# Kernel tuning notes

Measured on AMD Instinct MI355X. Metric: run time of the kernel, lower is better.

The kernel has to match this reference:

```python
import jax, jax.numpy as jnp
import numpy as np
from jax import lax

B, N = 4, 5  # batches, cavs per batch (record_len fixed to 5)
SHAPES = [(64, 128, 256), (128, 64, 128), (256, 32, 64)]  # (C,H,W) per scale


def _base_grid(H, W, align_corners):
    if align_corners:
        xs = jnp.linspace(-1.0, 1.0, W)
        ys = jnp.linspace(-1.0, 1.0, H)
    else:
        xs = (jnp.arange(W, dtype=jnp.float32) + 0.5) * (2.0 / W) - 1.0
        ys = (jnp.arange(H, dtype=jnp.float32) + 0.5) * (2.0 / H) - 1.0
    gx, gy = jnp.meshgrid(xs, ys)  # [H,W] each, x varies along W
    return jnp.stack([gx, gy], axis=-1)  # [H,W,2]


def affine_grid(theta, H, W, align_corners):
    # theta: [M,2,3]  -> grid [M,H,W,2], matches torch.F.affine_grid
    base = _base_grid(H, W, align_corners)
    coords = jnp.concatenate([base, jnp.ones((H, W, 1), base.dtype)], axis=-1)  # [H,W,3]
    return jnp.einsum('nij,hwj->nhwi', theta, coords)


def grid_sample(img, grid, align_corners):
    # img [M,C,H,W], grid [M,Hg,Wg,2]; bilinear, zero padding (torch defaults)
    M, C, H, W = img.shape
    gx, gy = grid[..., 0], grid[..., 1]
    if align_corners:
        ix = (gx + 1.0) * 0.5 * (W - 1)
        iy = (gy + 1.0) * 0.5 * (H - 1)
    else:
        ix = ((gx + 1.0) * W - 1.0) * 0.5
        iy = ((gy + 1.0) * H - 1.0) * 0.5
    x0 = jnp.floor(ix); y0 = jnp.floor(iy)
    x1 = x0 + 1.0;      y1 = y0 + 1.0
    wx1 = ix - x0; wx0 = 1.0 - wx1
    wy1 = iy - y0; wy0 = 1.0 - wy1

    def sample_corner(im, xx, yy):
        valid = ((xx >= 0) & (xx < W) & (yy >= 0) & (yy < H)).astype(im.dtype)
        xc = jnp.clip(xx, 0, W - 1).astype(jnp.int32)
        yc = jnp.clip(yy, 0, H - 1).astype(jnp.int32)
        return im[:, yc, xc] * valid[None]  # [C,Hg,Wg]

    def per_image(im, x0_, x1_, y0_, y1_, w00, w01, w10, w11):
        return (sample_corner(im, x0_, y0_) * w00[None]
                + sample_corner(im, x1_, y0_) * w01[None]
                + sample_corner(im, x0_, y1_) * w10[None]
                + sample_corner(im, x1_, y1_) * w11[None])

    return jax.vmap(per_image)(img, x0, x1, y0, y1, wx0 * wy0, wx1 * wy0, wx0 * wy1, wx1 * wy1)


def conv2d(x, w, b, pad):
    y = lax.conv_general_dilated(x, w, (1, 1), [(pad, pad), (pad, pad)],
                                 dimension_numbers=('NCHW', 'OIHW', 'NCHW'))
    return y + b[None, :, None, None]


def instance_norm(x, eps=1e-5):  # torch InstanceNorm2d(affine=False)
    m = jnp.mean(x, axis=(2, 3), keepdims=True)
    v = jnp.var(x, axis=(2, 3), keepdims=True)
    return (x - m) * lax.rsqrt(v + eps)


def leaky(x):
    return jnp.where(x >= 0, x, 0.01 * x)


def setup_inputs():
    key = jax.random.key(0)
    ks = jax.random.split(key, 8)
    out = {}
    for i, (C, H, W) in enumerate(SHAPES):
        out[f'feat{i}'] = jax.random.normal(ks[i], (B * N, C, H, W), dtype=jnp.float32)
    eye = jnp.array([[1., 0., 0.], [0., 1., 0.]], dtype=jnp.float32)
    out['pairwise_t_matrix'] = (jnp.broadcast_to(eye, (B, N, N, 2, 3))
                                + 0.02 * jax.random.normal(ks[3], (B, N, N, 2, 3), dtype=jnp.float32))
    out['record_len'] = jnp.full((B,), N, dtype=jnp.int32)
    C0 = SHAPES[0][0]
    def w(k, shape, fan):
        return jax.random.normal(k, shape, jnp.float32) * (1.0 / np.sqrt(fan))
    out['w1'] = w(ks[4], (32, 2 * C0, 3, 3), 2 * C0 * 9); out['b1'] = jnp.zeros((32,), jnp.float32)
    out['w2'] = w(ks[5], (16, 32, 3, 3), 32 * 9);          out['b2'] = jnp.zeros((16,), jnp.float32)
    out['w3'] = w(ks[6], (8, 16, 1, 1), 16);               out['b3'] = jnp.zeros((8,), jnp.float32)
    out['w4'] = w(ks[7], (2, 8, 1, 1), 8) * 0.1;           out['b4'] = jnp.zeros((2,), jnp.float32)
    return out


def _forward(feat0, feat1, feat2, pairwise_t_matrix, w1, b1, w2, b2, w3, b3, w4, b4):
    feats = [feat0, feat1, feat2]
    # warp every agent into ego (i=0) frame at every scale; warp_affine_simple uses align_corners=True
    theta = pairwise_t_matrix[:, 0, :, :, :].reshape(B * N, 2, 3)
    warped = []
    for f in feats:
        C, H, W = f.shape[1:]
        g = affine_grid(theta, H, W, True)
        warped.append(grid_sample(f, g, True).reshape(B, N, C, H, W))
    C0, H0, W0 = feats[0].shape[1:]
    w0 = warped[0]
    ego = jnp.broadcast_to(w0[:, :1], (B, N - 1, C0, H0, W0))
    cat = jnp.concatenate([ego, w0[:, 1:]], axis=2).reshape(B * (N - 1), 2 * C0, H0, W0)
    # ArbitraryOffset grid net
    x = leaky(instance_norm(conv2d(cat, w1, b1, 1)))
    x = leaky(instance_norm(conv2d(x, w2, b2, 1)))
    x = leaky(instance_norm(conv2d(x, w3, b3, 0)))
    x = conv2d(x, w4, b4, 0)  # [M,2,H0,W0]
    grid_res = x.reshape(B * (N - 1), H0, W0, 2)  # faithful: raw reshape as in the torch source
    grid = grid_res + _base_grid(H0, W0, False)   # identity affine_grid (align_corners=False)
    fused = []
    for s, f in enumerate(warped):
        C, Hs, Ws = f.shape[2:]
        gs = grid[:, ::2 ** s, ::2 ** s, :]  # [M,Hs,Ws,2]
        neigh = f[:, 1:].reshape(B * (N - 1), C, Hs, Ws)
        deformed = grid_sample(neigh, gs, False).reshape(B, N - 1, C, Hs, Ws)
        fused.append(jnp.max(jnp.concatenate([deformed, f[:, :1]], axis=1), axis=1))
    return tuple(fused)


def reference(feat0, feat1, feat2, pairwise_t_matrix, record_len, w1, b1, w2, b2, w3, b3, w4, b4):
    # record_len is fixed to N per batch (constant); kept for signature fidelity
    return _forward(feat0, feat1, feat2, pairwise_t_matrix, w1, b1, w2, b2, w3, b3, w4, b4)
```

## Files before the change

### kernel.cpp

```cpp
#include <hip/hip_runtime.h>


struct Bilin { int i00, i01, i10, i11; float w00, w01, w10, w11; };

__device__ __forceinline__ Bilin make_bilin(float ix, float iy, int W, int H) {
    float x0f = floorf(ix), y0f = floorf(iy);
    float wx1 = ix - x0f, wy1 = iy - y0f;
    float wx0 = 1.f - wx1, wy0 = 1.f - wy1;
    int x0 = (int)x0f, y0 = (int)y0f;
    int x1 = x0 + 1, y1 = y0 + 1;
    bool vx0 = (x0 >= 0 && x0 < W), vx1 = (x1 >= 0 && x1 < W);
    bool vy0 = (y0 >= 0 && y0 < H), vy1 = (y1 >= 0 && y1 < H);
    int cx0 = min(max(x0, 0), W - 1), cx1 = min(max(x1, 0), W - 1);
    int cy0 = min(max(y0, 0), H - 1), cy1 = min(max(y1, 0), H - 1);
    Bilin b;
    b.i00 = cy0 * W + cx0; b.i01 = cy0 * W + cx1;
    b.i10 = cy1 * W + cx0; b.i11 = cy1 * W + cx1;
    b.w00 = (vx0 && vy0) ? wx0 * wy0 : 0.f;
    b.w01 = (vx1 && vy0) ? wx1 * wy0 : 0.f;
    b.w10 = (vx0 && vy1) ? wx0 * wy1 : 0.f;
    b.w11 = (vx1 && vy1) ? wx1 * wy1 : 0.f;
    return b;
}

__device__ __forceinline__ Bilin affine_bilin(const float* th, int xq, int yq, int W, int H) {
    float gx = -1.f + 2.f * xq / (float)(W - 1);
    float gy = -1.f + 2.f * yq / (float)(H - 1);
    float tx = th[0] * gx + th[1] * gy + th[2];
    float ty = th[3] * gx + th[4] * gy + th[5];
    float ix = (tx + 1.f) * 0.5f * (W - 1);
    float iy = (ty + 1.f) * 0.5f * (H - 1);
    return make_bilin(ix, iy, W, H);
}

__global__ __launch_bounds__(256) void warp_kernel(
    const float* __restrict__ src, const float* __restrict__ tmat,
    float* __restrict__ dst, int C, int H, int W)
{
    int idx = blockIdx.x * 256 + threadIdx.x;
    int CGn = C >> 4;
    int HW = H * W;
    int total = 20 * CGn * HW;
    if (idx >= total) return;
    int w   = idx % W;
    int h   = (idx / W) % H;
    int cg  = (idx / HW) % CGn;
    int img = idx / (HW * CGn);
    int b = img / 5, n = img % 5;
    const float* th = tmat + (b * 25 + n) * 6;
    float gx = -1.f + 2.f * w / (float)(W - 1);
    float gy = -1.f + 2.f * h / (float)(H - 1);
    float tx = th[0] * gx + th[1] * gy + th[2];
    float ty = th[3] * gx + th[4] * gy + th[5];
    float ix = (tx + 1.f) * 0.5f * (W - 1);
    float iy = (ty + 1.f) * 0.5f * (H - 1);
    Bilin bl = make_bilin(ix, iy, W, H);
    const float* im = src + ((size_t)img * C + cg * 16) * HW;
    float* op = dst + ((size_t)img * C + cg * 16) * HW + h * W + w;
    #pragma unroll 4
    for (int c = 0; c < 16; ++c) {
        const float* pl = im + c * HW;
        op[c * HW] = pl[bl.i00] * bl.w00 + pl[bl.i01] * bl.w01 +
                     pl[bl.i10] * bl.w10 + pl[bl.i11] * bl.w11;
    }
}

__global__ void zero_stats(float* s) {
    for (int i = threadIdx.x; i < 1792; i += 256) s[i] = 0.f;
}

__global__ void finalize_stats(float* s, int n, float inv_hw) {
    int i = threadIdx.x;
    if (i < n) {
        float m = s[2 * i] * inv_hw;
        float v = s[2 * i + 1] * inv_hw - m * m;
        s[2 * i]     = m;
        s[2 * i + 1] = rsqrtf(v + 1e-5f);
    }
}

__global__ void transpose_w(const float* __restrict__ w1, const float* __restrict__ w2,
                            float* __restrict__ wt1, float* __restrict__ wt2) {
    int t = blockIdx.x * 256 + threadIdx.x;
    for (int i = t; i < 128 * 9 * 32; i += 32 * 256) {
        int o = i % 32, pos = (i / 32) % 9, cin = i / 288;
        wt1[i] = w1[o * 1152 + cin * 9 + pos];
    }
    for (int i = t; i < 32 * 9 * 16; i += 32 * 256) {
        int o = i % 16, pos = (i / 16) % 9, cin = i / 144;
        wt2[i] = w2[o * 288 + cin * 9 + pos];
    }
}

template<int CIN, int COUT, int SRC, bool INIT, bool NORM, bool STATS>
__global__ __launch_bounds__(256, 2) void conv3x3v3(
    const float* __restrict__ src, const float* __restrict__ wt,
    const float* __restrict__ bias, const float* __restrict__ stats,
    const float* __restrict__ init, float* __restrict__ dst,
    float* __restrict__ statacc)
{
    constexpr int H = 128, W = 256, HW = H * W;
    constexpr int CHUNK = 8, NCH = CIN / CHUNK;
    constexpr int OCP = COUT / 4;
    constexpr int PW = 68;
    __shared__ __align__(16) float s_in[CHUNK][10][PW];

    int tid = threadIdx.x, bi = blockIdx.x;
    int p = bi >> 6, rem = bi & 63;
    int h_base = (rem >> 2) * 8;
    int w_base = (rem & 3) * 64;
    int cg = tid >> 6, sg = tid & 63;
    int r = sg & 7, cw = (sg >> 3) * 8;
    int cg_u = __builtin_amdgcn_readfirstlane(cg);

    const float* base;
    if (SRC == 1)      base = src + (size_t)(p * 5) * 64 * HW;
    else if (SRC == 2) { int bb = p >> 2, jm = p & 3; base = src + (size_t)((bb * 5 + 1 + jm) * 64) * HW; }
    else               base = src + (size_t)p * CIN * HW;

    int gofs[3], lofs[3];
    unsigned pvm = 0, ivm = 0;
    #pragma unroll
    for (int k = 0; k < 3; ++k) {
        int e = tid + k * 256;
        bool pv = (e < 660);
        int row = e / 66, col = e % 66;
        int gy = h_base + row - 1, gx = w_base + col - 1;
        bool iv = pv && gy >= 0 && gy < H && gx >= 0 && gx < W;
        gofs[k] = iv ? (gy * W + gx) : 0;
        lofs[k] = pv ? (row * PW + col) : 0;
        pvm |= (pv ? 1u : 0u) << k;
        ivm |= (iv ? 1u : 0u) << k;
    }
    float* lds = &s_in[0][0][0];

    float acc[OCP][8];
    #pragma unroll
    for (int o = 0; o < OCP; ++o)
        #pragma unroll
        for (int i = 0; i < 8; ++i) acc[o][i] = 0.f;

    float pf[3][CHUNK];
    #pragma unroll
    for (int k = 0; k < 3; ++k)
        if (pvm >> k & 1)
            #pragma unroll
            for (int c = 0; c < CHUNK; ++c)
                pf[k][c] = base[(size_t)c * HW + gofs[k]];

    for (int ci = 0; ci < NCH; ++ci) {
        if (ci) __syncthreads();
        float mrs[NORM ? 2 * CHUNK : 1];
        if (NORM) {
            const float4* sp = (const float4*)(stats + (size_t)(p * CIN + ci * CHUNK) * 2);
            #pragma unroll
            for (int q = 0; q < CHUNK / 2; ++q) {
                float4 v = sp[q];
                mrs[q * 4] = v.x; mrs[q * 4 + 1] = v.y; mrs[q * 4 + 2] = v.z; mrs[q * 4 + 3] = v.w;
            }
        }
        #pragma unroll
        for (int k = 0; k < 3; ++k) {
            if (pvm >> k & 1) {
                #pragma unroll
                for (int c = 0; c < CHUNK; ++c) {
                    float v = (ivm >> k & 1) ? pf[k][c] : 0.f;
                    if (NORM && (ivm >> k & 1)) {
                        v = (v - mrs[2 * c]) * mrs[2 * c + 1];
                        v = v >= 0.f ? v : 0.01f * v;
                    }
                    lds[c * (10 * PW) + lofs[k]] = v;
                }
            }
        }
        __syncthreads();
        if (ci + 1 < NCH) {
            const float* nb = base + (size_t)(ci + 1) * CHUNK * HW;
            #pragma unroll
            for (int k = 0; k < 3; ++k)
                if (pvm >> k & 1)
                    #pragma unroll
                    for (int c = 0; c < CHUNK; ++c)
                        pf[k][c] = nb[(size_t)c * HW + gofs[k]];
        }
        #pragma unroll 1
        for (int c = 0; c < CHUNK; ++c) {
            float in[3][10];
            #pragma unroll
            for (int dy = 0; dy < 3; ++dy) {
                const float* rp = &s_in[c][r + dy][cw];
                float4 a = *reinterpret_cast<const float4*>(rp);
                float4 b = *reinterpret_cast<const float4*>(rp + 4);
                float2 e = *reinterpret_cast<const float2*>(rp + 8);
                in[dy][0] = a.x; in[dy][1] = a.y; in[dy][2] = a.z; in[dy][3] = a.w;
                in[dy][4] = b.x; in[dy][5] = b.y; in[dy][6] = b.z; in[dy][7] = b.w;
                in[dy][8] = e.x; in[dy][9] = e.y;
            }
            const float* wp = wt + (size_t)((ci * CHUNK + c) * 9) * COUT + cg_u * OCP;
            #pragma unroll
            for (int pos = 0; pos < 9; ++pos) {
                const int dy = pos / 3, dx = pos % 3;
                float wv[OCP];
                #pragma unroll
                for (int oq = 0; oq < OCP; oq += 4) {
                    float4 wq = *reinterpret_cast<const float4*>(wp + pos * COUT + oq);
                    wv[oq] = wq.x; wv[oq + 1] = wq.y; wv[oq + 2] = wq.z; wv[oq + 3] = wq.w;
                }
                #pragma unroll
                for (int o = 0; o < OCP; ++o)
                    #pragma unroll
                    for (int px = 0; px < 8; ++px)
                        acc[o][px] = fmaf(in[dy][dx + px], wv[o], acc[o][px]);
            }
        }
    }
    int hh = h_base + r, ww = w_base + cw;
    #pragma unroll
    for (int o = 0; o < OCP; ++o) {
        int oc = cg * OCP + o;
        float bv = (SRC == 1) ? 0.f : bias[oc];
        float add[8];
        #pragma unroll
        for (int i = 0; i < 8; ++i) add[i] = bv;
        if (INIT) {
            int bb = (SRC == 2) ? (p >> 2) : p;
            const float* ip = init + ((size_t)bb * COUT + oc) * HW + hh * W + ww;
            float4 e0 = *reinterpret_cast<const float4*>(ip);
            float4 e1 = *reinterpret_cast<const float4*>(ip + 4);
            add[0] += e0.x; add[1] += e0.y; add[2] += e0.z; add[3] += e0.w;
            add[4] += e1.x; add[5] += e1.y; add[6] += e1.z; add[7] += e1.w;
        }
        float vals[8];
        #pragma unroll
        for (int i = 0; i < 8; ++i) vals[i] = acc[o][i] + add[i];
        float* op = dst + (((size_t)p * COUT + oc) * H + hh) * W + ww;
        *reinterpret_cast<float4*>(op)     = make_float4(vals[0], vals[1], vals[2], vals[3]);
        *reinterpret_cast<float4*>(op + 4) = make_float4(vals[4], vals[5], vals[6], vals[7]);
        if (STATS) {
            float s = 0.f, s2 = 0.f;
            #pragma unroll
            for (int i = 0; i < 8; ++i) { s += vals[i]; s2 += vals[i] * vals[i]; }
            #pragma unroll
            for (int off = 32; off > 0; off >>= 1) {
                s  += __shfl_down(s, off);
                s2 += __shfl_down(s2, off);
            }
            if (sg == 0) {
                atomicAdd(&statacc[(size_t)(p * COUT + oc) * 2],     s);
                atomicAdd(&statacc[(size_t)(p * COUT + oc) * 2 + 1], s2);
            }
        }
    }
}

template<int CIN, int COUT, bool STATS>
__global__ __launch_bounds__(256) void conv1x1_kernel(
    const float* __restrict__ src, const float* __restrict__ wgt,
    const float* __restrict__ bias, const float* __restrict__ stats,
    float* __restrict__ dst, float* __restrict__ statacc)
{
    constexpr int HW = 128 * 256;
    __shared__ float s_w[COUT * CIN];
    __shared__ float s_b[COUT];
    __shared__ float s_part[4][2 * COUT];
    int tid = threadIdx.x;
    for (int t = tid; t < COUT * CIN; t += 256) s_w[t] = wgt[t];
    if (tid < COUT) s_b[tid] = bias[tid];
    __syncthreads();
    int p  = blockIdx.x >> 7;
    int px = ((blockIdx.x & 127) << 8) + tid;
    float in[CIN];
    #pragma unroll
    for (int c = 0; c < CIN; ++c) {
        float v  = src[((size_t)p * CIN + c) * HW + px];
        float m  = stats[(p * CIN + c) * 2];
        float rs = stats[(p * CIN + c) * 2 + 1];
        v = (v - m) * rs;
        in[c] = v >= 0.f ? v : 0.01f * v;
    }
    float val[COUT];
    #pragma unroll
    for (int o = 0; o < COUT; ++o) {
        float s = s_b[o];
        #pragma unroll
        for (int c = 0; c < CIN; ++c) s = fmaf(in[c], s_w[o * CIN + c], s);
        val[o] = s;
        dst[((size_t)p * COUT + o) * HW + px] = s;
    }
    if (STATS) {
        int wv = tid >> 6, ln = tid & 63;
        #pragma unroll
        for (int o = 0; o < COUT; ++o) {
            float s = val[o], s2 = val[o] * val[o];
            #pragma unroll
            for (int off = 32; off > 0; off >>= 1) {
                s  += __shfl_down(s, off);
                s2 += __shfl_down(s2, off);
            }
            if (ln == 0) { s_part[wv][o * 2] = s; s_part[wv][o * 2 + 1] = s2; }
        }
        __syncthreads();
        if (tid < 2 * COUT) {
            float t = s_part[0][tid] + s_part[1][tid] + s_part[2][tid] + s_part[3][tid];
            atomicAdd(&statacc[(size_t)p * COUT * 2 + tid], t);
        }
    }
}

__global__ __launch_bounds__(256) void fuse0_kernel(
    const float* __restrict__ W0, const float* __restrict__ grid,
    float* __restrict__ out)
{
    constexpr int HW = 32768;
    constexpr int CPT = 16;
    int bid = blockIdx.x;
    int swz = (bid & 7) * 256 + (bid >> 3);
    int idx = swz * 256 + threadIdx.x;
    int px = idx & 32767;
    int cg = (idx >> 15) & 3;
    int b  = idx >> 17;
    int w = px & 255, h = px >> 8;
    float bx = (w + 0.5f) * (2.f / 256.f) - 1.f;
    float by = (h + 0.5f) * (2.f / 128.f) - 1.f;
    Bilin bl[4];
    #pragma unroll
    for (int j = 0; j < 4; ++j) {
        const float2 g = *reinterpret_cast<const float2*>(
            grid + ((size_t)(b * 4 + j)) * 65536 + (size_t)px * 2);
        float ix = ((g.x + bx + 1.f) * 256.f - 1.f) * 0.5f;
        float iy = ((g.y + by + 1.f) * 128.f - 1.f) * 0.5f;
        bl[j] = make_bilin(ix, iy, 256, 128);
    }
    const float* ego = W0 + ((size_t)(b * 5) * 64 + cg * CPT) * HW + px;
    float* op = out + ((size_t)b * 64 + cg * CPT) * HW + px;
    #pragma unroll 2
    for (int c = 0; c < CPT; ++c) {
        float mx = ego[(size_t)c * HW];
        #pragma unroll
        for (int j = 0; j < 4; ++j) {
            const float* pl = W0 + ((size_t)(b * 5 + 1 + j) * 64 + cg * CPT + c) * HW;
            float s = pl[bl[j].i00] * bl[j].w00 + pl[bl[j].i01] * bl[j].w01 +
                      pl[bl[j].i10] * bl[j].w10 + pl[bl[j].i11] * bl[j].w11;
            mx = fmaxf(mx, s);
        }
        op[(size_t)c * HW] = mx;
    }
}

template<int C, int CPT, int SH, int HS, int WS>
__global__ __launch_bounds__(256) void fuse_comp(
    const float* __restrict__ feat, const float* __restrict__ tmat,
    const float* __restrict__ grid, float* __restrict__ out)
{
    constexpr int HW = HS * WS;
    constexpr int NCG = C / CPT;
    int idx = blockIdx.x * 256 + threadIdx.x;
    if (idx >= 4 * NCG * HW) return;
    int px = idx % HW;
    int cg = (idx / HW) % NCG;
    int b  = idx / (HW * NCG);
    int w = px % WS, h = px / WS;

    float m[CPT];
    {
        const float* th = tmat + (size_t)(b * 25) * 6;
        float t0 = th[0], t1 = th[1], t2 = th[2], t3 = th[3], t4 = th[4], t5 = th[5];
        float thr[6] = {t0, t1, t2, t3, t4, t5};
        Bilin bi = affine_bilin(thr, w, h, WS, HS);
        const float* pb = feat + ((size_t)(b * 5) * C + cg * CPT) * HW;
        #pragma unroll 4
        for (int c = 0; c < CPT; ++c) {
            const float* pl = pb + (size_t)c * HW;
            m[c] = pl[bi.i00] * bi.w00 + pl[bi.i01] * bi.w01 +
                   pl[bi.i10] * bi.w10 + pl[bi.i11] * bi.w11;
        }
    }
    int h0 = h << SH, w0 = w << SH;
    float bx = (w0 + 0.5f) * (2.f / 256.f) - 1.f;
    float by = (h0 + 0.5f) * (2.f / 128.f) - 1.f;
    for (int j = 0; j < 4; ++j) {
        const float2 g = *reinterpret_cast<const float2*>(
            grid + ((size_t)(b * 4 + j)) * 65536 + (size_t)(h0 * 256 + w0) * 2);
        float ix = ((g.x + bx + 1.f) * WS - 1.f) * 0.5f;
        float iy = ((g.y + by + 1.f) * HS - 1.f) * 0.5f;
        float x0f = floorf(ix), y0f = floorf(iy);
        float wx1 = ix - x0f, wy1 = iy - y0f;
        float wx0 = 1.f - wx1, wy0 = 1.f - wy1;
        int x0 = (int)x0f, y0 = (int)y0f, x1 = x0 + 1, y1 = y0 + 1;
        bool vx0 = (x0 >= 0 && x0 < WS), vx1 = (x1 >= 0 && x1 < WS);
        bool vy0 = (y0 >= 0 && y0 < HS), vy1 = (y1 >= 0 && y1 < HS);
        int cx0 = min(max(x0, 0), WS - 1), cx1 = min(max(x1, 0), WS - 1);
        int cy0 = min(max(y0, 0), HS - 1), cy1 = min(max(y1, 0), HS - 1);
        float ow[4] = { (vx0 && vy0) ? wx0 * wy0 : 0.f,
                        (vx1 && vy0) ? wx1 * wy0 : 0.f,
                        (vx0 && vy1) ? wx0 * wy1 : 0.f,
                        (vx1 && vy1) ? wx1 * wy1 : 0.f };
        int qx[4] = { cx0, cx1, cx0, cx1 };
        int qy[4] = { cy0, cy0, cy1, cy1 };
        const float* th = tmat + (size_t)(b * 25 + 1 + j) * 6;
        float thr[6] = { th[0], th[1], th[2], th[3], th[4], th[5] };
        Bilin in_[4];
        #pragma unroll
        for (int q = 0; q < 4; ++q) {
            in_[q] = affine_bilin(thr, qx[q], qy[q], WS, HS);
            in_[q].w00 *= ow[q]; in_[q].w01 *= ow[q];
            in_[q].w10 *= ow[q]; in_[q].w11 *= ow[q];
        }
        const float* pb = feat + ((size_t)(b * 5 + 1 + j) * C + cg * CPT) * HW;
        #pragma unroll 2
        for (int c = 0; c < CPT; ++c) {
            const float* pl = pb + (size_t)c * HW;
            float s = 0.f;
            #pragma unroll
            for (int q = 0; q < 4; ++q)
                s += pl[in_[q].i00] * in_[q].w00 + pl[in_[q].i01] * in_[q].w01 +
                     pl[in_[q].i10] * in_[q].w10 + pl[in_[q].i11] * in_[q].w11;
            m[c] = fmaxf(m[c], s);
        }
    }
    float* op = out + ((size_t)b * C + cg * CPT) * HW + px;
    #pragma unroll
    for (int c = 0; c < CPT; ++c) op[(size_t)c * HW] = m[c];
}

extern "C" void kernel_launch(void* const* d_in, const int* in_sizes, int n_in,
                              void* d_out, int out_size, void* d_ws, size_t ws_size,
                              hipStream_t stream)
{
    const float* feat0 = (const float*)d_in[0];
    const float* feat1 = (const float*)d_in[1];
    const float* feat2 = (const float*)d_in[2];
    const float* tmat  = (const float*)d_in[3];
    const float* w1 = (const float*)d_in[5];
    const float* b1 = (const float*)d_in[6];
    const float* w2 = (const float*)d_in[7];
    const float* b2 = (const float*)d_in[8];
    const float* w3 = (const float*)d_in[9];
    const float* b3 = (const float*)d_in[10];
    const float* w4 = (const float*)d_in[11];
    const float* b4 = (const float*)d_in[12];
    float* out = (float*)d_out;
    float* ws  = (float*)d_ws;

    const size_t nW0 = 41943040;
    const size_t nX1 = 16777216;
    const size_t nX2 = 8388608;
    const size_t nX3 = 4194304;
    const size_t nG  = 2097152;
    const size_t nS  = 2048;
    const size_t nWT = 36864 + 4608;
    const size_t needed = (nW0 + nX1 + nX2 + nX3 + nG + nS + nWT) * 4;
    if (ws_size < needed) return;

    float* W0  = ws;
    float* X1  = W0 + nW0;
    float* X2  = X1 + nX1;
    float* X3  = X2 + nX2;
    float* G   = X3 + nX3;
    float* S   = G  + nG;
    float* WT1 = S  + nS;
    float* WT2 = WT1 + 36864;
    float* E   = X2;

    zero_stats<<<1, 256, 0, stream>>>(S);
    transpose_w<<<32, 256, 0, stream>>>(w1, w2, WT1, WT2);

    warp_kernel<<<10240, 256, 0, stream>>>(feat0, tmat, W0, 64, 128, 256);

    conv3x3v3<64, 32, 1, false, false, false><<<256,  256, 0, stream>>>(W0, WT1, b1, nullptr, nullptr, E, nullptr);
    conv3x3v3<64, 32, 2, true,  false, true ><<<1024, 256, 0, stream>>>(W0, WT1 + 8 * 8 * 9 * 32, b1, nullptr, E, X1, S);
    finalize_stats<<<1, 512, 0, stream>>>(S, 512, 1.f / 32768.f);
    conv3x3v3<32, 16, 0, false, true,  true ><<<1024, 256, 0, stream>>>(X1, WT2, b2, S, nullptr, X2, S + 1024);
    finalize_stats<<<1, 256, 0, stream>>>(S + 1024, 256, 1.f / 32768.f);
    conv1x1_kernel<16, 8, true ><<<2048, 256, 0, stream>>>(X2, w3, b3, S + 1024, X3, S + 1536);
    finalize_stats<<<1, 128, 0, stream>>>(S + 1536, 128, 1.f / 32768.f);
    conv1x1_kernel<8, 2, false><<<2048, 256, 0, stream>>>(X3, w4, b4, S + 1536, G, nullptr);

    fuse0_kernel<<<2048, 256, 0, stream>>>(W0, G, out);
    fuse_comp<128, 32, 1, 64, 128><<<512, 256, 0, stream>>>(feat1, tmat, G, out + 8388608);
    fuse_comp<256, 16, 2, 32,  64><<<512, 256, 0, stream>>>(feat2, tmat, G, out + 12582912);
}
```

Baseline: 1.356 ms.

## Stage conv weights in LDS with double-buffered reads; swizzle and split fuse_comp blocks

The 3x3 conv kernel now copies each chunk's weight slice into shared memory and reads weights from there instead of global memory. Weight vectors are double-buffered across the 9 tap positions, and input rows are loaded lazily to overlap LDS reads with FMAs. fuse_comp halves channels per thread, doubles the grid, and swizzles block indices to spread batches and channel groups across CUs. Extra LDS per block may reduce occupancy of the 2-blocks-per-CU conv.

```diff
diff --git a/kernel.cpp b/kernel.cpp
--- a/kernel.cpp
+++ b/kernel.cpp
@@ -92,8 +92,17 @@
     }
 }
 
+__device__ __forceinline__ void load_row10(float* d, const float* rp) {
+    float4 a = *reinterpret_cast<const float4*>(rp);
+    float4 b = *reinterpret_cast<const float4*>(rp + 4);
+    float2 e = *reinterpret_cast<const float2*>(rp + 8);
+    d[0] = a.x; d[1] = a.y; d[2] = a.z; d[3] = a.w;
+    d[4] = b.x; d[5] = b.y; d[6] = b.z; d[7] = b.w;
+    d[8] = e.x; d[9] = e.y;
+}
+
 template<int CIN, int COUT, int SRC, bool INIT, bool NORM, bool STATS>
-__global__ __launch_bounds__(256, 2) void conv3x3v3(
+__global__ __launch_bounds__(256, 2) void conv3x3v4(
     const float* __restrict__ src, const float* __restrict__ wt,
     const float* __restrict__ bias, const float* __restrict__ stats,
     const float* __restrict__ init, float* __restrict__ dst,
@@ -102,8 +111,11 @@
     constexpr int H = 128, W = 256, HW = H * W;
     constexpr int CHUNK = 8, NCH = CIN / CHUNK;
     constexpr int OCP = COUT / 4;
+    constexpr int WQN = OCP / 4;
     constexpr int PW = 68;
+    constexpr int WSLICE = CHUNK * 9 * COUT;
     __shared__ __align__(16) float s_in[CHUNK][10][PW];
+    __shared__ __align__(16) float s_w[WSLICE];
 
     int tid = threadIdx.x, bi = blockIdx.x;
     int p = bi >> 6, rem = bi & 63;
@@ -173,6 +185,10 @@
                 }
             }
         }
+        {
+            const float* wsl = wt + (size_t)ci * WSLICE;
+            for (int t = tid; t < WSLICE; t += 256) s_w[t] = wsl[t];
+        }
         __syncthreads();
         if (ci + 1 < NCH) {
             const float* nb = base + (size_t)(ci + 1) * CHUNK * HW;
@@ -185,26 +201,31 @@
         }
         #pragma unroll 1
         for (int c = 0; c < CHUNK; ++c) {
+            const float* swp = s_w + (size_t)(c * 9) * COUT + cg_u * OCP;
+            float4 wq[2][WQN];
+            #pragma unroll
+            for (int q = 0; q < WQN; ++q)
+                wq[0][q] = *reinterpret_cast<const float4*>(swp + q * 4);
             float in[3][10];
-            #pragma unroll
-            for (int dy = 0; dy < 3; ++dy) {
-                const float* rp = &s_in[c][r + dy][cw];
-                float4 a = *reinterpret_cast<const float4*>(rp);
-                float4 b = *reinterpret_cast<const float4*>(rp + 4);
-                float2 e = *reinterpret_cast<const float2*>(rp + 8);
-                in[dy][0] = a.x; in[dy][1] = a.y; in[dy][2] = a.z; in[dy][3] = a.w;
-                in[dy][4] = b.x; in[dy][5] = b.y; in[dy][6] = b.z; in[dy][7] = b.w;
-                in[dy][8] = e.x; in[dy][9] = e.y;
-            }
-            const float* wp = wt + (size_t)((ci * CHUNK + c) * 9) * COUT + cg_u * OCP;
+            load_row10(&in[0][0], &s_in[c][r][cw]);
             #pragma unroll
             for (int pos = 0; pos < 9; ++pos) {
                 const int dy = pos / 3, dx = pos % 3;
+                if (pos < 8) {
+                    const float* np = swp + (pos + 1) * COUT;
+                    #pragma unroll
+                    for (int q = 0; q < WQN; ++q)
+                        wq[(pos + 1) & 1][q] = *reinterpret_cast<const float4*>(np + q * 4);
+                }
+                if (pos == 1) load_row10(&in[1][0], &s_in[c][r + 1][cw]);
+                if (pos == 4) load_row10(&in[2][0], &s_in[c][r + 2][cw]);
                 float wv[OCP];
                 #pragma unroll
-                for (int oq = 0; oq < OCP; oq += 4) {
-                    float4 wq = *reinterpret_cast<const float4*>(wp + pos * COUT + oq);
-                    wv[oq] = wq.x; wv[oq + 1] = wq.y; wv[oq + 2] = wq.z; wv[oq + 3] = wq.w;
+                for (int q = 0; q < WQN; ++q) {
+                    wv[q * 4]     = wq[pos & 1][q].x;
+                    wv[q * 4 + 1] = wq[pos & 1][q].y;
+                    wv[q * 4 + 2] = wq[pos & 1][q].z;
+                    wv[q * 4 + 3] = wq[pos & 1][q].w;
                 }
                 #pragma unroll
                 for (int o = 0; o < OCP; ++o)
@@ -354,7 +375,10 @@
 {
     constexpr int HW = HS * WS;
     constexpr int NCG = C / CPT;
-    int idx = blockIdx.x * 256 + threadIdx.x;
+    constexpr int NBLK = 4 * NCG * HW / 256;
+    int bid = blockIdx.x;
+    int swz = (bid & 7) * (NBLK / 8) + (bid >> 3);
+    int idx = swz * 256 + threadIdx.x;
     if (idx >= 4 * NCG * HW) return;
     int px = idx % HW;
     int cg = (idx / HW) % NCG;
@@ -467,16 +491,16 @@
 
     warp_kernel<<<10240, 256, 0, stream>>>(feat0, tmat, W0, 64, 128, 256);
 
-    conv3x3v3<64, 32, 1, false, false, false><<<256,  256, 0, stream>>>(W0, WT1, b1, nullptr, nullptr, E, nullptr);
-    conv3x3v3<64, 32, 2, true,  false, true ><<<1024, 256, 0, stream>>>(W0, WT1 + 8 * 8 * 9 * 32, b1, nullptr, E, X1, S);
+    conv3x3v4<64, 32, 1, false, false, false><<<256,  256, 0, stream>>>(W0, WT1, b1, nullptr, nullptr, E, nullptr);
+    conv3x3v4<64, 32, 2, true,  false, true ><<<1024, 256, 0, stream>>>(W0, WT1 + 8 * 8 * 9 * 32, b1, nullptr, E, X1, S);
     finalize_stats<<<1, 512, 0, stream>>>(S, 512, 1.f / 32768.f);
-    conv3x3v3<32, 16, 0, false, true,  true ><<<1024, 256, 0, stream>>>(X1, WT2, b2, S, nullptr, X2, S + 1024);
+    conv3x3v4<32, 16, 0, false, true,  true ><<<1024, 256, 0, stream>>>(X1, WT2, b2, S, nullptr, X2, S + 1024);
     finalize_stats<<<1, 256, 0, stream>>>(S + 1024, 256, 1.f / 32768.f);
     conv1x1_kernel<16, 8, true ><<<2048, 256, 0, stream>>>(X2, w3, b3, S + 1024, X3, S + 1536);
     finalize_stats<<<1, 128, 0, stream>>>(S + 1536, 128, 1.f / 32768.f);
     conv1x1_kernel<8, 2, false><<<2048, 256, 0, stream>>>(X3, w4, b4, S + 1536, G, nullptr);
 
     fuse0_kernel<<<2048, 256, 0, stream>>>(W0, G, out);
-    fuse_comp<128, 32, 1, 64, 128><<<512, 256, 0, stream>>>(feat1, tmat, G, out + 8388608);
-    fuse_comp<256, 16, 2, 32,  64><<<512, 256, 0, stream>>>(feat2, tmat, G, out + 12582912);
-}
+    fuse_comp<128, 16, 1, 64, 128><<<1024, 256, 0, stream>>>(feat1, tmat, G, out + 8388608);
+    fuse_comp<256, 8, 2, 32,  64><<<1024, 256, 0, stream>>>(feat2, tmat, G, out + 12582912);
+}
```

After: 1.399 ms. 3.1% more time.
